# Performance work log

Hardware: AMD Instinct MI355X
Metric: run time of the kernel (lower is better)

Reference implementation:

```python
import jax, jax.numpy as jnp
import numpy as np

D_MODEL = 64
D_STATE = 16
D_CONV = 4
EXPAND = 2
D_INNER = EXPAND * D_MODEL        # 128
DT_RANK = max(1, D_MODEL // 16)   # 4 (mamba_ssm default ceil(d_model/16))
BATCH, HH, WW = 2, 128, 128


def setup_inputs() -> dict:
    key = jax.random.key(0)
    ks = jax.random.split(key, 10)
    def norm(k, shape, sc=0.05):
        return jax.random.normal(k, shape, jnp.float32) * sc
    # A initialized as in mamba_ssm: A = 1..d_state per channel, stored as log
    A_log = jnp.log(jnp.tile(jnp.arange(1, D_STATE + 1, dtype=jnp.float32), (4, D_INNER, 1)))
    return {
        "x": jax.random.normal(ks[0], (BATCH, D_MODEL, HH, WW), jnp.float32),
        "in_w": norm(ks[1], (4, 2 * D_INNER, D_MODEL)),
        "conv_w": norm(ks[2], (4, D_INNER, D_CONV), 0.2),
        "conv_b": jnp.zeros((4, D_INNER), jnp.float32),
        "xp_w": norm(ks[3], (4, DT_RANK + 2 * D_STATE, D_INNER)),
        "dtp_w": norm(ks[4], (4, D_INNER, DT_RANK), 0.2),
        "dtp_b": jnp.full((4, D_INNER), -4.0, jnp.float32) + norm(ks[5], (4, D_INNER), 0.5),
        "A_log": A_log,
        "Dp": jnp.ones((4, D_INNER), jnp.float32),
        "out_w": norm(ks[6], (4, D_MODEL, D_INNER)),
        "fuse_w": norm(ks[7], (D_MODEL, 4 * D_MODEL)),
        "fuse_b": jnp.zeros((D_MODEL,), jnp.float32),
        "ln_g": jnp.ones((D_MODEL,), jnp.float32),
        "ln_b": jnp.zeros((D_MODEL,), jnp.float32),
    }


def _mamba(xseq, in_w, conv_w, conv_b, xp_w, dtp_w, dtp_b, A_log, Dp, out_w):
    # xseq: (N, L, d_model) -> (N, L, d_model). Single-direction Mamba block.
    N, L, _ = xseq.shape
    xz = xseq @ in_w.T                       # (N, L, 2*d_inner)
    u, z = jnp.split(xz, 2, axis=-1)
    # causal depthwise conv1d, kernel width D_CONV
    up = jnp.pad(u, ((0, 0), (D_CONV - 1, 0), (0, 0)))
    uc = conv_b + sum(up[:, k:k + L, :] * conv_w[:, k][None, None, :] for k in range(D_CONV))
    uc = jax.nn.silu(uc)
    dbl = uc @ xp_w.T                        # (N, L, dt_rank + 2*d_state)
    dt = jax.nn.softplus(dbl[..., :DT_RANK] @ dtp_w.T + dtp_b)   # (N, L, d_inner)
    Bm = dbl[..., DT_RANK:DT_RANK + D_STATE]                     # (N, L, d_state)
    Cm = dbl[..., DT_RANK + D_STATE:]                            # (N, L, d_state)
    A = -jnp.exp(A_log)                                          # (d_inner, d_state)

    def step(h, inp):
        dt_t, B_t, C_t, u_t = inp            # (N,d_inner),(N,d_state),(N,d_state),(N,d_inner)
        h = h * jnp.exp(dt_t[..., None] * A) + (dt_t * u_t)[..., None] * B_t[:, None, :]
        y = jnp.einsum('nds,ns->nd', h, C_t)
        return h, y

    h0 = jnp.zeros((N, D_INNER, D_STATE), xseq.dtype)
    _, ys = jax.lax.scan(step, h0, (dt.swapaxes(0, 1), Bm.swapaxes(0, 1),
                                    Cm.swapaxes(0, 1), uc.swapaxes(0, 1)))
    y = ys.swapaxes(0, 1) + uc * Dp
    y = y * jax.nn.silu(z)
    return y @ out_w.T


def reference(x, in_w, conv_w, conv_b, xp_w, dtp_w, dtp_b, A_log, Dp, out_w,
              fuse_w, fuse_b, ln_g, ln_b):
    B, C, H, W = x.shape
    xhwc = x.transpose(0, 2, 3, 1)           # (B,H,W,C)
    xwhc = x.transpose(0, 3, 2, 1)           # (B,W,H,C)
    d0 = xhwc.reshape(B * H, W, C)                         # horizontal fwd
    d1 = xhwc[:, :, ::-1, :].reshape(B * H, W, C)          # horizontal bwd
    d2 = xwhc.reshape(B * W, H, C)                         # vertical fwd
    d3 = xwhc[:, :, ::-1, :].reshape(B * W, H, C)          # vertical bwd
    xd = jnp.stack([d0, d1, d2, d3])         # (4, B*S, S, C) since H == W
    ys = jax.vmap(_mamba)(xd, in_w, conv_w, conv_b, xp_w, dtp_w, dtp_b, A_log, Dp, out_w)
    y0 = ys[0].reshape(B, H, W, C)
    y1 = ys[1].reshape(B, H, W, C)[:, :, ::-1, :]
    y2 = ys[2].reshape(B, W, H, C).transpose(0, 2, 1, 3)
    y3 = ys[3].reshape(B, W, H, C)[:, :, ::-1, :].transpose(0, 2, 1, 3)
    cat = jnp.concatenate([y0, y1, y2, y3], axis=-1)       # (B,H,W,4C)
    f = cat @ fuse_w.T + fuse_b                            # 1x1 conv
    mu = f.mean(-1, keepdims=True)
    var = f.var(-1, keepdims=True)
    f = (f - mu) * jax.lax.rsqrt(var + 1e-5) * ln_g + ln_b # LayerNorm over C
    f = jax.nn.silu(f)
    return f.transpose(0, 3, 1, 2)                          # (B,C,H,W)
```

## Files before the change

### kernel.cpp

```cpp
#include <hip/hip_runtime.h>
#include <math.h>


typedef __attribute__((ext_vector_type(8))) short short8;
typedef __attribute__((ext_vector_type(4))) float f32x4;

__device__ __forceinline__ unsigned short f2bf(float f) {
  unsigned int u = __float_as_uint(f);
  u += 0x7fffu + ((u >> 16) & 1u);
  return (unsigned short)(u >> 16);
}
__device__ __forceinline__ float bf2f(unsigned short h) {
  return __uint_as_float(((unsigned int)h) << 16);
}
__device__ __forceinline__ float siluf(float x) { return x / (1.f + __expf(-x)); }

__global__ void k0_prep(const float* __restrict__ out_w, const float* __restrict__ fuse_w,
                        const float* __restrict__ in_w, const float* __restrict__ xp_w,
                        unsigned short* __restrict__ MT16, unsigned short* __restrict__ W16,
                        unsigned short* __restrict__ XW16) {
  int blk = blockIdx.x;
  int tid = threadIdx.x;
  if (blk < 128) {
    int idx = blk * 256 + tid;
    int d   = idx & 127;
    int o   = (idx >> 7) & 63;
    int dir = idx >> 13;
    float acc = 0.f;
    #pragma unroll 8
    for (int j = 0; j < 64; ++j)
      acc += out_w[(dir*64 + j)*128 + d] * fuse_w[o*256 + dir*64 + j];
    MT16[o*512 + dir*128 + d] = f2bf(acc);
  } else if (blk < 160) {
    int t = (blk - 128) * 256 + tid;
    int base = t * 8;
    float4 v0 = *(const float4*)(in_w + base);
    float4 v1 = *(const float4*)(in_w + base + 4);
    uint4 pk;
    pk.x = (unsigned int)f2bf(v0.x) | ((unsigned int)f2bf(v0.y) << 16);
    pk.y = (unsigned int)f2bf(v0.z) | ((unsigned int)f2bf(v0.w) << 16);
    pk.z = (unsigned int)f2bf(v1.x) | ((unsigned int)f2bf(v1.y) << 16);
    pk.w = (unsigned int)f2bf(v1.z) | ((unsigned int)f2bf(v1.w) << 16);
    *(uint4*)(W16 + base) = pk;
  } else {
    int t = (blk - 160) * 256 + tid;
    for (int pid = t; pid < 4*48*128; pid += 1024) {
      int dir = pid / 6144;
      int rem = pid - dir*6144;
      int row = rem >> 7, c = rem & 127;
      XW16[pid] = (row < 36) ? f2bf(xp_w[dir*4608 + row*128 + c]) : (unsigned short)0;
    }
  }
}

__global__ __launch_bounds__(256, 3) void k1_front(
    const float* __restrict__ x,
    const unsigned short* __restrict__ W16, const unsigned short* __restrict__ XW16,
    const float* __restrict__ conv_w, const float* __restrict__ conv_b,
    const float* __restrict__ dtp_w, const float* __restrict__ dtp_b,
    const float* __restrict__ A_log, const float* __restrict__ Dp,
    unsigned short* __restrict__ ZB, unsigned short* __restrict__ YF)
{
  __shared__ __align__(16) char smem[53248];
  unsigned short* sxb = (unsigned short*)smem;
  float* sBCf         = (float*)smem;
  unsigned short* sUC = (unsigned short*)(smem + 18432);

  const int tid = threadIdx.x;
  const int dir = blockIdx.x >> 8;
  const int n   = blockIdx.x & 255;
  const int b   = n >> 7;
  const int r   = n & 127;
  const float* xb = x + (size_t)b * (64*128*128);
  const int n_all = dir*256 + n;
  unsigned short* ZBn = ZB + (size_t)n_all * 16384;

  if (dir == 0) {
    for (int f = tid*4; f < 8192; f += 1024) {
      int c = f >> 7, l = f & 127;
      float4 v = *(const float4*)(xb + ((size_t)c*128 + r)*128 + l);
      sxb[(l+0)*72 + c] = f2bf(v.x);
      sxb[(l+1)*72 + c] = f2bf(v.y);
      sxb[(l+2)*72 + c] = f2bf(v.z);
      sxb[(l+3)*72 + c] = f2bf(v.w);
    }
  } else if (dir == 1) {
    for (int f = tid*4; f < 8192; f += 1024) {
      int c = f >> 7, w = f & 127;
      float4 v = *(const float4*)(xb + ((size_t)c*128 + r)*128 + w);
      sxb[(127-w)*72 + c] = f2bf(v.x);
      sxb[(126-w)*72 + c] = f2bf(v.y);
      sxb[(125-w)*72 + c] = f2bf(v.z);
      sxb[(124-w)*72 + c] = f2bf(v.w);
    }
  } else if (dir == 2) {
    for (int f = tid; f < 8192; f += 256) {
      int c = f >> 7, l = f & 127;
      sxb[l*72 + c] = f2bf(xb[((size_t)c*128 + l)*128 + r]);
    }
  } else {
    for (int f = tid; f < 8192; f += 256) {
      int c = f >> 7, l = f & 127;
      sxb[l*72 + c] = f2bf(xb[((size_t)c*128 + (127-l))*128 + r]);
    }
  }
  __syncthreads();

  {
    const int wave = tid >> 6;
    const int lane = tid & 63;
    const int m16 = lane & 15;
    const int quad = lane >> 4;
    const int tb0 = wave * 32;

    short8 bfr[2][2];
    #pragma unroll
    for (int tt = 0; tt < 2; ++tt)
      #pragma unroll
      for (int ks = 0; ks < 2; ++ks)
        bfr[tt][ks] = *(const short8*)(sxb + (tb0 + tt*16 + m16)*72 + ks*32 + quad*8);

    const unsigned short* Wd = W16 + (size_t)dir * 16384;

    for (int rt = 0; rt < 16; ++rt) {
      short8 af[2];
      #pragma unroll
      for (int ks = 0; ks < 2; ++ks)
        af[ks] = *(const short8*)(Wd + (rt*16 + m16)*64 + ks*32 + quad*8);
      #pragma unroll
      for (int tt = 0; tt < 2; ++tt) {
        f32x4 acc = {0.f, 0.f, 0.f, 0.f};
        acc = __builtin_amdgcn_mfma_f32_16x16x32_bf16(af[0], bfr[tt][0], acc, 0, 0, 0);
        acc = __builtin_amdgcn_mfma_f32_16x16x32_bf16(af[1], bfr[tt][1], acc, 0, 0, 0);
        const int tok = tb0 + tt*16 + m16;
        const int r0 = rt*16 + quad*4;
        if (rt < 8) {
          uint2 u2;
          u2.x = (unsigned int)f2bf(acc[0]) | ((unsigned int)f2bf(acc[1]) << 16);
          u2.y = (unsigned int)f2bf(acc[2]) | ((unsigned int)f2bf(acc[3]) << 16);
          *(uint2*)(sUC + tok*136 + r0) = u2;
        } else {
          uint2 u2;
          u2.x = (unsigned int)f2bf(siluf(acc[0])) | ((unsigned int)f2bf(siluf(acc[1])) << 16);
          u2.y = (unsigned int)f2bf(siluf(acc[2])) | ((unsigned int)f2bf(siluf(acc[3])) << 16);
          *(uint2*)(ZBn + (size_t)tok*128 + (r0 - 128)) = u2;
        }
      }
    }
  }
  __syncthreads();

  {
    const int d = tid & 127;
    const int half = tid >> 7;
    const int lc0 = half * 64;
    const float* cw = conv_w + (size_t)(dir*128 + d)*4;
    const float c0w = cw[0], c1w = cw[1], c2w = cw[2], c3w = cw[3];
    const float cb = conv_b[dir*128 + d];
    float p0 = half ? bf2f(sUC[(lc0-3)*136 + d]) : 0.f;
    float p1 = half ? bf2f(sUC[(lc0-2)*136 + d]) : 0.f;
    float p2 = half ? bf2f(sUC[(lc0-1)*136 + d]) : 0.f;
    __syncthreads();
    for (int l = lc0; l < lc0 + 64; ++l) {
      float cur = bf2f(sUC[l*136 + d]);
      float v = cb + c0w*p0 + c1w*p1 + c2w*p2 + c3w*cur;
      sUC[l*136 + d] = f2bf(siluf(v));
      p0 = p1; p1 = p2; p2 = cur;
    }
  }
  __syncthreads();

  {
    const int wave = tid >> 6;
    const int lane = tid & 63;
    const int m16 = lane & 15;
    const int quad = lane >> 4;
    const int tb0 = wave * 32;

    short8 bfr[2][4];
    #pragma unroll
    for (int tt = 0; tt < 2; ++tt)
      #pragma unroll
      for (int ks = 0; ks < 4; ++ks)
        bfr[tt][ks] = *(const short8*)(sUC + (tb0 + tt*16 + m16)*136 + ks*32 + quad*8);

    const unsigned short* XWd = XW16 + (size_t)dir * (48*128);

    for (int rt = 0; rt < 3; ++rt) {
      short8 af[4];
      #pragma unroll
      for (int ks = 0; ks < 4; ++ks)
        af[ks] = *(const short8*)(XWd + (rt*16 + m16)*128 + ks*32 + quad*8);
      #pragma unroll
      for (int tt = 0; tt < 2; ++tt) {
        f32x4 acc = {0.f, 0.f, 0.f, 0.f};
        #pragma unroll
        for (int ks = 0; ks < 4; ++ks)
          acc = __builtin_amdgcn_mfma_f32_16x16x32_bf16(af[ks], bfr[tt][ks], acc, 0, 0, 0);
        const int tok = tb0 + tt*16 + m16;
        const int r0 = rt*16 + quad*4;
        if (r0 == 0) {
          float4 v; v.x = acc[0]; v.y = acc[1]; v.z = acc[2]; v.w = acc[3];
          *(float4*)(smem + 18432 + tok*272 + 256) = v;
        } else if (r0 < 36) {
          float4 v; v.x = acc[0]; v.y = acc[1]; v.z = acc[2]; v.w = acc[3];
          *(float4*)(sBCf + tok*36 + (r0 - 4)) = v;
        }
      }
    }
  }
  __syncthreads();

  {
    const int d = tid >> 1;
    const int p = tid & 1;
    const float* dwp = dtp_w + (size_t)(dir*128 + d) * 4;
    const float dw0 = dwp[0], dw1 = dwp[1], dw2 = dwp[2], dw3 = dwp[3];
    const float db = dtp_b[dir*128 + d];
    const float dpv = Dp[dir*128 + d];

    float Av[8];
    bool fast = true;
    #pragma unroll
    for (int j = 0; j < 8; ++j) {
      float a = -__expf(A_log[((size_t)(dir*128 + d))*16 + p*8 + j]);
      Av[j] = a;
      if (fabsf((-a) - (float)(p*8 + j + 1)) > 1e-3f) fast = false;
    }

    float h[8];
    #pragma unroll
    for (int j = 0; j < 8; ++j) h[j] = 0.f;

    #define SCAN_LOAD                                                     \
      float4 q0 = *(const float4*)(smem + 18432 + l*272 + 256);           \
      float4 b0 = *(const float4*)(sBCf + l*36 + p*8);                    \
      float4 b1 = *(const float4*)(sBCf + l*36 + p*8 + 4);                \
      float4 c0 = *(const float4*)(sBCf + l*36 + 16 + p*8);               \
      float4 c1 = *(const float4*)(sBCf + l*36 + 16 + p*8 + 4);           \
      float Bv[8] = {b0.x,b0.y,b0.z,b0.w, b1.x,b1.y,b1.z,b1.w};           \
      float Cv[8] = {c0.x,c0.y,c0.z,c0.w, c1.x,c1.y,c1.z,c1.w};           \
      float dr = q0.x*dw0 + q0.y*dw1 + q0.z*dw2 + q0.w*dw3 + db;          \
      float dt = (dr > 20.f) ? dr : __logf(1.f + __expf(dr));             \
      float u = bf2f(sUC[l*136 + d]);                                     \
      float dtu = dt * u;

    if (fast) {
      for (int l = 0; l < 128; ++l) {
        SCAN_LOAD
        float E = __expf(-dt);
        float E2 = E*E, E4 = E2*E2, E8 = E4*E4;
        float e = p ? E8 : 1.f;
        float yp = 0.f;
        #pragma unroll
        for (int j = 0; j < 8; ++j) {
          e *= E;
          h[j] = h[j]*e + dtu*Bv[j];
          yp += h[j]*Cv[j];
        }
        float ysum = yp + __shfl_xor(yp, 1, 64);
        if (p == 0) sUC[l*136 + d] = f2bf(ysum + u*dpv);
      }
    } else {
      for (int l = 0; l < 128; ++l) {
        SCAN_LOAD
        float yp = 0.f;
        #pragma unroll
        for (int j = 0; j < 8; ++j) {
          float ej = __expf(dt*Av[j]);
          h[j] = h[j]*ej + dtu*Bv[j];
          yp += h[j]*Cv[j];
        }
        float ysum = yp + __shfl_xor(yp, 1, 64);
        if (p == 0) sUC[l*136 + d] = f2bf(ysum + u*dpv);
      }
    }
    #undef SCAN_LOAD
  }
  __syncthreads();

  for (int f = tid*8; f < 16384; f += 2048) {
    int l = f >> 7, dz = f & 127;
    uint4 yv = *(const uint4*)(sUC + l*136 + dz);
    uint4 zv = *(const uint4*)(ZBn + f);
    const unsigned int* py = (const unsigned int*)&yv;
    const unsigned int* pz = (const unsigned int*)&zv;
    uint4 ov;
    unsigned int* po = (unsigned int*)&ov;
    #pragma unroll
    for (int q = 0; q < 4; ++q) {
      float ylo = __uint_as_float(py[q] << 16);
      float yhi = __uint_as_float(py[q] & 0xffff0000u);
      float zlo = __uint_as_float(pz[q] << 16);
      float zhi = __uint_as_float(pz[q] & 0xffff0000u);
      po[q] = (unsigned int)f2bf(ylo*zlo) | ((unsigned int)f2bf(yhi*zhi) << 16);
    }
    size_t oaddr;
    if (dir < 2)       oaddr = ((size_t)n_all*128 + l)*128 + dz;
    else if (dir == 2) oaddr = ((size_t)(512 + b*128 + l)*128 + r)*128 + dz;
    else               oaddr = ((size_t)(768 + b*128 + (127-l))*128 + r)*128 + dz;
    *(uint4*)(YF + oaddr) = ov;
  }
}

__global__ __launch_bounds__(256, 2) void k3_fuse(
    const unsigned short* __restrict__ YF, const unsigned short* __restrict__ MT16,
    const float* __restrict__ fuse_b, const float* __restrict__ ln_g,
    const float* __restrict__ ln_b, float* __restrict__ out)
{
  __shared__ __align__(16) unsigned short sYB[64*520];

  const int tid = threadIdx.x;
  const int blk = blockIdx.x;
  const int b = blk >> 8;
  const int rr2 = blk & 255;
  const int h = rr2 >> 1;
  const int w0 = (rr2 & 1) * 64;

  for (int f = tid*8; f < 32768; f += 2048) {
    int dirg = f >> 13;
    int rem = f & 8191;
    int tok = rem >> 7;
    int dd = rem & 127;
    int X = (dirg == 1) ? (127 - w0 - tok) : (w0 + tok);
    size_t base = ((size_t)(dirg*256 + b*128 + h)*128 + X)*128 + dd;
    *(uint4*)(sYB + tok*520 + dirg*128 + dd) = *(const uint4*)(YF + base);
  }
  __syncthreads();

  const int wave = tid >> 6;
  const int lane = tid & 63;
  const int m16 = lane & 15;
  const int quad = lane >> 4;
  const int tok = wave*16 + m16;

  short8 bfr[16];
  #pragma unroll
  for (int jt = 0; jt < 16; ++jt)
    bfr[jt] = *(const short8*)(sYB + tok*520 + jt*32 + quad*8);

  float facc[4][4];
  #pragma unroll
  for (int mt = 0; mt < 4; ++mt) {
    f32x4 acc = {0.f, 0.f, 0.f, 0.f};
    #pragma unroll
    for (int jt = 0; jt < 16; ++jt) {
      short8 af = *(const short8*)(MT16 + (size_t)(mt*16 + m16)*512 + jt*32 + quad*8);
      acc = __builtin_amdgcn_mfma_f32_16x16x32_bf16(af, bfr[jt], acc, 0, 0, 0);
    }
    facc[mt][0] = acc[0]; facc[mt][1] = acc[1]; facc[mt][2] = acc[2]; facc[mt][3] = acc[3];
  }

  float fv[16];
  float s1 = 0.f, s2 = 0.f;
  #pragma unroll
  for (int mt = 0; mt < 4; ++mt)
    #pragma unroll
    for (int rr = 0; rr < 4; ++rr) {
      int o = mt*16 + quad*4 + rr;
      float v = facc[mt][rr] + fuse_b[o];
      fv[mt*4 + rr] = v;
      s1 += v; s2 += v*v;
    }
  s1 += __shfl_xor(s1, 16, 64); s1 += __shfl_xor(s1, 32, 64);
  s2 += __shfl_xor(s2, 16, 64); s2 += __shfl_xor(s2, 32, 64);
  float mu = s1 * (1.f/64.f);
  float var = s2 * (1.f/64.f) - mu*mu;
  float rs = rsqrtf(var + 1e-5f);

  #pragma unroll
  for (int mt = 0; mt < 4; ++mt)
    #pragma unroll
    for (int rr = 0; rr < 4; ++rr) {
      int o = mt*16 + quad*4 + rr;
      float v = (fv[mt*4 + rr] - mu) * rs * ln_g[o] + ln_b[o];
      out[((size_t)(b*64 + o)*128 + h)*128 + (w0 + tok)] = siluf(v);
    }
}

extern "C" void kernel_launch(void* const* d_in, const int* in_sizes, int n_in,
                              void* d_out, int out_size, void* d_ws, size_t ws_size,
                              hipStream_t stream) {
  const float* x      = (const float*)d_in[0];
  const float* in_w   = (const float*)d_in[1];
  const float* conv_w = (const float*)d_in[2];
  const float* conv_b = (const float*)d_in[3];
  const float* xp_w   = (const float*)d_in[4];
  const float* dtp_w  = (const float*)d_in[5];
  const float* dtp_b  = (const float*)d_in[6];
  const float* A_log  = (const float*)d_in[7];
  const float* Dp     = (const float*)d_in[8];
  const float* out_w  = (const float*)d_in[9];
  const float* fuse_w = (const float*)d_in[10];
  const float* fuse_b = (const float*)d_in[11];
  const float* ln_g   = (const float*)d_in[12];
  const float* ln_b   = (const float*)d_in[13];
  float* out = (float*)d_out;

  char* ws = (char*)d_ws;
  unsigned short* ZB   = (unsigned short*)(ws);
  unsigned short* YF   = (unsigned short*)(ws + 33554432);
  unsigned short* MT16 = (unsigned short*)(ws + 67108864);
  unsigned short* W16  = (unsigned short*)(ws + 67174400);
  unsigned short* XW16 = (unsigned short*)(ws + 67305472);

  k0_prep<<<dim3(164), dim3(256), 0, stream>>>(out_w, fuse_w, in_w, xp_w, MT16, W16, XW16);
  k1_front<<<dim3(1024), dim3(256), 0, stream>>>(x, W16, XW16, conv_w, conv_b,
                                                 dtp_w, dtp_b, A_log, Dp, ZB, YF);
  k3_fuse<<<dim3(512), dim3(256), 0, stream>>>(YF, MT16, fuse_b, ln_g, ln_b, out);
}
```

Before: 243.7 us.

## Pre-transpose input to bf16 token-major layouts and keep gate z in registers

The input is now converted once to bf16 in two channel-last layouts (row-major and column-major) by extra prep work and a new transpose kernel. The front kernel then loads MFMA operands straight from global memory instead of doing strided fp32 gathers into shared memory, which were especially uncoalesced for the vertical directions. The SiLU-gated z half of the input projection is kept packed in registers and applied at the end, removing the ZB global round trip. This costs one extra kernel launch, an intermediate buffer, and higher register pressure in k1.

Measured after the change: 229.4 us. 1.06x faster.

```diff
diff --git a/kernel.cpp b/kernel.cpp
--- a/kernel.cpp
+++ b/kernel.cpp
@@ -17,8 +17,10 @@
 
 __global__ void k0_prep(const float* __restrict__ out_w, const float* __restrict__ fuse_w,
                         const float* __restrict__ in_w, const float* __restrict__ xp_w,
+                        const float* __restrict__ x,
                         unsigned short* __restrict__ MT16, unsigned short* __restrict__ W16,
-                        unsigned short* __restrict__ XW16) {
+                        unsigned short* __restrict__ XW16, unsigned short* __restrict__ XH) {
+  __shared__ unsigned short sT[64*132];
   int blk = blockIdx.x;
   int tid = threadIdx.x;
   if (blk < 128) {
@@ -42,7 +44,7 @@
     pk.z = (unsigned int)f2bf(v1.x) | ((unsigned int)f2bf(v1.y) << 16);
     pk.w = (unsigned int)f2bf(v1.z) | ((unsigned int)f2bf(v1.w) << 16);
     *(uint4*)(W16 + base) = pk;
-  } else {
+  } else if (blk < 164) {
     int t = (blk - 160) * 256 + tid;
     for (int pid = t; pid < 4*48*128; pid += 1024) {
       int dir = pid / 6144;
@@ -50,19 +52,54 @@
       int row = rem >> 7, c = rem & 127;
       XW16[pid] = (row < 36) ? f2bf(xp_w[dir*4608 + row*128 + c]) : (unsigned short)0;
     }
+  } else {
+    int idx = blk - 164;
+    int b = idx >> 7, h = idx & 127;
+    for (int f = tid*4; f < 8192; f += 1024) {
+      int c = f >> 7, w = f & 127;
+      float4 v = *(const float4*)(x + (((size_t)(b*64 + c)*128 + h)*128 + w));
+      sT[c*132 + w + 0] = f2bf(v.x);
+      sT[c*132 + w + 1] = f2bf(v.y);
+      sT[c*132 + w + 2] = f2bf(v.z);
+      sT[c*132 + w + 3] = f2bf(v.w);
+    }
+    __syncthreads();
+    for (int f = tid*8; f < 8192; f += 2048) {
+      int w = f >> 6, c0 = f & 63;
+      unsigned int pk[4];
+      #pragma unroll
+      for (int p = 0; p < 4; ++p) {
+        unsigned int lo = sT[(c0 + p*2 + 0)*132 + w];
+        unsigned int hi = sT[(c0 + p*2 + 1)*132 + w];
+        pk[p] = lo | (hi << 16);
+      }
+      uint4 v; v.x = pk[0]; v.y = pk[1]; v.z = pk[2]; v.w = pk[3];
+      *(uint4*)(XH + (((size_t)(b*128 + h)*128 + w)*64 + c0)) = v;
+    }
+  }
+}
+
+__global__ void kT2(const unsigned short* __restrict__ XH, unsigned short* __restrict__ XW) {
+  int idx = blockIdx.x;
+  int b = idx >> 7, h = idx & 127;
+  int tid = threadIdx.x;
+  const unsigned short* src = XH + ((size_t)(b*128 + h)*128)*64;
+  for (int f = tid*8; f < 8192; f += 2048) {
+    int w = f >> 6, c = f & 63;
+    uint4 v = *(const uint4*)(src + f);
+    *(uint4*)(XW + (((size_t)(b*128 + w)*128 + h)*64 + c)) = v;
   }
 }
 
 __global__ __launch_bounds__(256, 3) void k1_front(
-    const float* __restrict__ x,
+    const unsigned short* __restrict__ XH, const unsigned short* __restrict__ XW,
     const unsigned short* __restrict__ W16, const unsigned short* __restrict__ XW16,
     const float* __restrict__ conv_w, const float* __restrict__ conv_b,
     const float* __restrict__ dtp_w, const float* __restrict__ dtp_b,
     const float* __restrict__ A_log, const float* __restrict__ Dp,
-    unsigned short* __restrict__ ZB, unsigned short* __restrict__ YF)
+    unsigned short* __restrict__ YF)
 {
   __shared__ __align__(16) char smem[53248];
-  unsigned short* sxb = (unsigned short*)smem;
   float* sBCf         = (float*)smem;
   unsigned short* sUC = (unsigned short*)(smem + 18432);
 
@@ -71,58 +108,32 @@
   const int n   = blockIdx.x & 255;
   const int b   = n >> 7;
   const int r   = n & 127;
-  const float* xb = x + (size_t)b * (64*128*128);
   const int n_all = dir*256 + n;
-  unsigned short* ZBn = ZB + (size_t)n_all * 16384;
-
-  if (dir == 0) {
-    for (int f = tid*4; f < 8192; f += 1024) {
-      int c = f >> 7, l = f & 127;
-      float4 v = *(const float4*)(xb + ((size_t)c*128 + r)*128 + l);
-      sxb[(l+0)*72 + c] = f2bf(v.x);
-      sxb[(l+1)*72 + c] = f2bf(v.y);
-      sxb[(l+2)*72 + c] = f2bf(v.z);
-      sxb[(l+3)*72 + c] = f2bf(v.w);
-    }
-  } else if (dir == 1) {
-    for (int f = tid*4; f < 8192; f += 1024) {
-      int c = f >> 7, w = f & 127;
-      float4 v = *(const float4*)(xb + ((size_t)c*128 + r)*128 + w);
-      sxb[(127-w)*72 + c] = f2bf(v.x);
-      sxb[(126-w)*72 + c] = f2bf(v.y);
-      sxb[(125-w)*72 + c] = f2bf(v.z);
-      sxb[(124-w)*72 + c] = f2bf(v.w);
-    }
-  } else if (dir == 2) {
-    for (int f = tid; f < 8192; f += 256) {
-      int c = f >> 7, l = f & 127;
-      sxb[l*72 + c] = f2bf(xb[((size_t)c*128 + l)*128 + r]);
-    }
-  } else {
-    for (int f = tid; f < 8192; f += 256) {
-      int c = f >> 7, l = f & 127;
-      sxb[l*72 + c] = f2bf(xb[((size_t)c*128 + (127-l))*128 + r]);
-    }
-  }
-  __syncthreads();
+
+  const unsigned short* xsrc = (dir < 2 ? XH : XW) + ((size_t)(b*128 + r)*128)*64;
+
+  const int wave = tid >> 6;
+  const int lane = tid & 63;
+  const int m16 = lane & 15;
+  const int quad = lane >> 4;
+  const int tb0 = wave * 32;
+  const int st0 = tb0 + m16;
+  const int st1 = tb0 + 16 + m16;
+  const int sp0 = (dir & 1) ? (127 - st0) : st0;
+  const int sp1 = (dir & 1) ? (127 - st1) : st1;
+
+  unsigned int zpk[2][8][2];
 
   {
-    const int wave = tid >> 6;
-    const int lane = tid & 63;
-    const int m16 = lane & 15;
-    const int quad = lane >> 4;
-    const int tb0 = wave * 32;
-
     short8 bfr[2][2];
     #pragma unroll
-    for (int tt = 0; tt < 2; ++tt)
-      #pragma unroll
-      for (int ks = 0; ks < 2; ++ks)
-        bfr[tt][ks] = *(const short8*)(sxb + (tb0 + tt*16 + m16)*72 + ks*32 + quad*8);
-
+    for (int ks = 0; ks < 2; ++ks) {
+      bfr[0][ks] = *(const short8*)(xsrc + sp0*64 + ks*32 + quad*8);
+      bfr[1][ks] = *(const short8*)(xsrc + sp1*64 + ks*32 + quad*8);
+    }
     const unsigned short* Wd = W16 + (size_t)dir * 16384;
 
-    for (int rt = 0; rt < 16; ++rt) {
+    for (int rt = 0; rt < 8; ++rt) {
       short8 af[2];
       #pragma unroll
       for (int ks = 0; ks < 2; ++ks)
@@ -132,19 +143,27 @@
         f32x4 acc = {0.f, 0.f, 0.f, 0.f};
         acc = __builtin_amdgcn_mfma_f32_16x16x32_bf16(af[0], bfr[tt][0], acc, 0, 0, 0);
         acc = __builtin_amdgcn_mfma_f32_16x16x32_bf16(af[1], bfr[tt][1], acc, 0, 0, 0);
-        const int tok = tb0 + tt*16 + m16;
+        const int tok = tt ? st1 : st0;
         const int r0 = rt*16 + quad*4;
-        if (rt < 8) {
-          uint2 u2;
-          u2.x = (unsigned int)f2bf(acc[0]) | ((unsigned int)f2bf(acc[1]) << 16);
-          u2.y = (unsigned int)f2bf(acc[2]) | ((unsigned int)f2bf(acc[3]) << 16);
-          *(uint2*)(sUC + tok*136 + r0) = u2;
-        } else {
-          uint2 u2;
-          u2.x = (unsigned int)f2bf(siluf(acc[0])) | ((unsigned int)f2bf(siluf(acc[1])) << 16);
-          u2.y = (unsigned int)f2bf(siluf(acc[2])) | ((unsigned int)f2bf(siluf(acc[3])) << 16);
-          *(uint2*)(ZBn + (size_t)tok*128 + (r0 - 128)) = u2;
-        }
+        uint2 u2;
+        u2.x = (unsigned int)f2bf(acc[0]) | ((unsigned int)f2bf(acc[1]) << 16);
+        u2.y = (unsigned int)f2bf(acc[2]) | ((unsigned int)f2bf(acc[3]) << 16);
+        *(uint2*)(sUC + tok*136 + r0) = u2;
+      }
+    }
+    #pragma unroll
+    for (int k = 0; k < 8; ++k) {
+      short8 af[2];
+      #pragma unroll
+      for (int ks = 0; ks < 2; ++ks)
+        af[ks] = *(const short8*)(Wd + ((8+k)*16 + m16)*64 + ks*32 + quad*8);
+      #pragma unroll
+      for (int tt = 0; tt < 2; ++tt) {
+        f32x4 acc = {0.f, 0.f, 0.f, 0.f};
+        acc = __builtin_amdgcn_mfma_f32_16x16x32_bf16(af[0], bfr[tt][0], acc, 0, 0, 0);
+        acc = __builtin_amdgcn_mfma_f32_16x16x32_bf16(af[1], bfr[tt][1], acc, 0, 0, 0);
+        zpk[tt][k][0] = (unsigned int)f2bf(siluf(acc[0])) | ((unsigned int)f2bf(siluf(acc[1])) << 16);
+        zpk[tt][k][1] = (unsigned int)f2bf(siluf(acc[2])) | ((unsigned int)f2bf(siluf(acc[3])) << 16);
       }
     }
   }
@@ -171,18 +190,12 @@
   __syncthreads();
 
   {
-    const int wave = tid >> 6;
-    const int lane = tid & 63;
-    const int m16 = lane & 15;
-    const int quad = lane >> 4;
-    const int tb0 = wave * 32;
-
     short8 bfr[2][4];
     #pragma unroll
     for (int tt = 0; tt < 2; ++tt)
       #pragma unroll
       for (int ks = 0; ks < 4; ++ks)
-        bfr[tt][ks] = *(const short8*)(sUC + (tb0 + tt*16 + m16)*136 + ks*32 + quad*8);
+        bfr[tt][ks] = *(const short8*)(sUC + (tt ? st1 : st0)*136 + ks*32 + quad*8);
 
     const unsigned short* XWd = XW16 + (size_t)dir * (48*128);
 
@@ -197,7 +210,7 @@
         #pragma unroll
         for (int ks = 0; ks < 4; ++ks)
           acc = __builtin_amdgcn_mfma_f32_16x16x32_bf16(af[ks], bfr[tt][ks], acc, 0, 0, 0);
-        const int tok = tb0 + tt*16 + m16;
+        const int tok = tt ? st1 : st0;
         const int r0 = rt*16 + quad*4;
         if (r0 == 0) {
           float4 v; v.x = acc[0]; v.y = acc[1]; v.z = acc[2]; v.w = acc[3];
@@ -279,27 +292,31 @@
   }
   __syncthreads();
 
-  for (int f = tid*8; f < 16384; f += 2048) {
-    int l = f >> 7, dz = f & 127;
-    uint4 yv = *(const uint4*)(sUC + l*136 + dz);
-    uint4 zv = *(const uint4*)(ZBn + f);
-    const unsigned int* py = (const unsigned int*)&yv;
-    const unsigned int* pz = (const unsigned int*)&zv;
-    uint4 ov;
-    unsigned int* po = (unsigned int*)&ov;
-    #pragma unroll
-    for (int q = 0; q < 4; ++q) {
-      float ylo = __uint_as_float(py[q] << 16);
-      float yhi = __uint_as_float(py[q] & 0xffff0000u);
-      float zlo = __uint_as_float(pz[q] << 16);
-      float zhi = __uint_as_float(pz[q] & 0xffff0000u);
-      po[q] = (unsigned int)f2bf(ylo*zlo) | ((unsigned int)f2bf(yhi*zhi) << 16);
-    }
-    size_t oaddr;
-    if (dir < 2)       oaddr = ((size_t)n_all*128 + l)*128 + dz;
-    else if (dir == 2) oaddr = ((size_t)(512 + b*128 + l)*128 + r)*128 + dz;
-    else               oaddr = ((size_t)(768 + b*128 + (127-l))*128 + r)*128 + dz;
-    *(uint4*)(YF + oaddr) = ov;
+  #pragma unroll
+  for (int tt = 0; tt < 2; ++tt) {
+    const int st = tt ? st1 : st0;
+    size_t rowbase;
+    if (dir < 2)       rowbase = ((size_t)n_all*128 + st)*128;
+    else if (dir == 2) rowbase = ((size_t)(512 + b*128 + st)*128 + r)*128;
+    else               rowbase = ((size_t)(768 + b*128 + (127-st))*128 + r)*128;
+    #pragma unroll
+    for (int k = 0; k < 8; ++k) {
+      const int dz = 16*k + quad*4;
+      uint2 yv = *(const uint2*)(sUC + st*136 + dz);
+      float y0 = __uint_as_float(yv.x << 16);
+      float y1 = __uint_as_float(yv.x & 0xffff0000u);
+      float y2 = __uint_as_float(yv.y << 16);
+      float y3 = __uint_as_float(yv.y & 0xffff0000u);
+      unsigned int z01 = zpk[tt][k][0], z23 = zpk[tt][k][1];
+      float z0 = __uint_as_float(z01 << 16);
+      float z1 = __uint_as_float(z01 & 0xffff0000u);
+      float z2 = __uint_as_float(z23 << 16);
+      float z3 = __uint_as_float(z23 & 0xffff0000u);
+      uint2 ov;
+      ov.x = (unsigned int)f2bf(y0*z0) | ((unsigned int)f2bf(y1*z1) << 16);
+      ov.y = (unsigned int)f2bf(y2*z2) | ((unsigned int)f2bf(y3*z3) << 16);
+      *(uint2*)(YF + rowbase + dz) = ov;
+    }
   }
 }
 
@@ -398,14 +415,17 @@
   float* out = (float*)d_out;
 
   char* ws = (char*)d_ws;
-  unsigned short* ZB   = (unsigned short*)(ws);
-  unsigned short* YF   = (unsigned short*)(ws + 33554432);
-  unsigned short* MT16 = (unsigned short*)(ws + 67108864);
-  unsigned short* W16  = (unsigned short*)(ws + 67174400);
-  unsigned short* XW16 = (unsigned short*)(ws + 67305472);
-
-  k0_prep<<<dim3(164), dim3(256), 0, stream>>>(out_w, fuse_w, in_w, xp_w, MT16, W16, XW16);
-  k1_front<<<dim3(1024), dim3(256), 0, stream>>>(x, W16, XW16, conv_w, conv_b,
-                                                 dtp_w, dtp_b, A_log, Dp, ZB, YF);
+  unsigned short* YF   = (unsigned short*)(ws);
+  unsigned short* MT16 = (unsigned short*)(ws + 33554432);
+  unsigned short* W16  = (unsigned short*)(ws + 33619968);
+  unsigned short* XW16 = (unsigned short*)(ws + 33751040);
+  unsigned short* XH   = (unsigned short*)(ws + 33800192);
+  unsigned short* XWt  = (unsigned short*)(ws + 37994496);
+
+  k0_prep<<<dim3(420), dim3(256), 0, stream>>>(out_w, fuse_w, in_w, xp_w, x,
+                                               MT16, W16, XW16, XH);
+  kT2<<<dim3(256), dim3(256), 0, stream>>>(XH, XWt);
+  k1_front<<<dim3(1024), dim3(256), 0, stream>>>(XH, XWt, W16, XW16, conv_w, conv_b,
+                                                 dtp_w, dtp_b, A_log, Dp, YF);
   k3_fuse<<<dim3(512), dim3(256), 0, stream>>>(YF, MT16, fuse_b, ln_g, ln_b, out);
 }
```
